# Optimization experiments

Hardware: AMD Instinct MI355X
Metric: run time of the kernel (lower is better)

Reference implementation:

```python
import jax, jax.numpy as jnp
import numpy as np

D_MODEL = 1024
NUM_HEADS = 16
D_K = D_MODEL // NUM_HEADS
THETA = 10000.0


def _rope(x, pos):
    # x: [H, B, S, D_K]; pos: [S] int. Interleaved-pair rotation (matrix-form RoPE).
    d2 = D_K // 2
    inv_freq = THETA ** (-(2.0 * jnp.arange(d2, dtype=jnp.float32)) / D_K)  # [d2]
    ang = pos.astype(jnp.float32)[:, None] * inv_freq[None, :]              # [S, d2]
    sin, cos = jnp.sin(ang), jnp.cos(ang)
    xr = x.reshape(*x.shape[:-1], d2, 2)
    x0, x1 = xr[..., 0], xr[..., 1]
    out0 = cos * x0 - sin * x1
    out1 = sin * x0 + cos * x1
    return jnp.stack([out0, out1], axis=-1).reshape(x.shape)


def setup_inputs() -> dict:
    key = jax.random.key(0)
    ks = jax.random.split(key, 5)
    scale = 1.0 / np.sqrt(D_MODEL)
    return {
        "x": jax.random.normal(ks[0], (4, 2048, D_MODEL), dtype=jnp.float32),
        "token_positions": jnp.arange(2048, dtype=jnp.int32),
        "Wq": jax.random.normal(ks[1], (D_MODEL, D_MODEL), dtype=jnp.float32) * scale,
        "Wk": jax.random.normal(ks[2], (D_MODEL, D_MODEL), dtype=jnp.float32) * scale,
        "Wv": jax.random.normal(ks[3], (D_MODEL, D_MODEL), dtype=jnp.float32) * scale,
        "Wo": jax.random.normal(ks[4], (D_MODEL, D_MODEL), dtype=jnp.float32) * scale,
    }


def reference(x, token_positions, Wq, Wk, Wv, Wo):
    B, S, D = x.shape
    H, dk = NUM_HEADS, D_K
    # Projections (Linear stores weight [out,in], applies x @ W.T)
    def proj(W):
        return (x @ W.T).reshape(B, S, H, dk).transpose(2, 0, 1, 3)  # [H,B,S,dk]
    q, k, v = proj(Wq), proj(Wk), proj(Wv)
    q = _rope(q, token_positions)
    k = _rope(k, token_positions)
    scores = jnp.einsum("hbsd,hbtd->hbst", q, k) / jnp.sqrt(jnp.float32(dk))
    causal = jnp.tril(jnp.ones((S, S), dtype=bool))
    scores = jnp.where(causal, scores, jnp.float32(-1e9))
    attn = jax.nn.softmax(scores, axis=-1)
    out = jnp.einsum("hbst,hbtd->hbsd", attn, v)       # [H,B,S,dk]
    out = out.transpose(1, 2, 0, 3).reshape(B, S, D)   # [B,S,D]
    return out @ Wo.T
```

## Files before the change

kernel.cpp:

```cpp
#include <hip/hip_runtime.h>

typedef __bf16 bf16;
typedef bf16 bf16x8 __attribute__((ext_vector_type(8)));
typedef bf16 bf16x4 __attribute__((ext_vector_type(4)));
typedef float floatx4 __attribute__((ext_vector_type(4)));

#define D_MODEL 1024
#define SEQ     2048
#define NB      4
#define NH      16
#define DKH     64
#define ROPE_L2 0.4152410118609203f

__device__ __forceinline__ floatx4 mfma16(bf16x8 a, bf16x8 b, floatx4 c) {
  return __builtin_amdgcn_mfma_f32_16x16x32_bf16(a, b, c, 0, 0, 0);
}

__device__ __forceinline__ void gload_lds16(void* lds_uniform, const void* gsrc) {
  __builtin_amdgcn_global_load_lds(
      (__attribute__((address_space(1))) unsigned int*)(void*)(gsrc),
      (__attribute__((address_space(3))) unsigned int*)lds_uniform,
      16, 0, 0);
}

__global__ __launch_bounds__(256) void cvt_all(
    const float4* __restrict__ x,
    const float4* __restrict__ wq, const float4* __restrict__ wk,
    const float4* __restrict__ wv, const float4* __restrict__ wo,
    bf16x4* __restrict__ xb,
    bf16x4* __restrict__ b0, bf16x4* __restrict__ b1,
    bf16x4* __restrict__ b2, bf16x4* __restrict__ b3,
    const int* __restrict__ tokpos, float2* __restrict__ ropetab) {
  const int i = blockIdx.x * 256 + threadIdx.x;
  if (i < (1 << 21) + (1 << 20)) {
    const float4* src;
    bf16x4* dst;
    int off;
    if (i < (1 << 21)) {
      src = x; dst = xb; off = i;
    } else {
      const int j = i - (1 << 21);
      const int widx = j >> 18;
      off = j & ((1 << 18) - 1);
      src = (widx == 0) ? wq : (widx == 1) ? wk : (widx == 2) ? wv : wo;
      dst = (widx == 0) ? b0 : (widx == 1) ? b1 : (widx == 2) ? b2 : b3;
    }
    const float4 v = src[off];
    bf16x4 o;
    o[0] = (bf16)v.x; o[1] = (bf16)v.y; o[2] = (bf16)v.z; o[3] = (bf16)v.w;
    dst[off] = o;
  } else {
    const int k = i - (1 << 21) - (1 << 20);
    const int s = k >> 5, i2 = k & 31;
    const float ang = (float)tokpos[s] * exp2f(-(float)i2 * ROPE_L2);
    float sn, cs;
    sincosf(ang, &sn, &cs);
    ropetab[k] = make_float2(sn, cs);
  }
}

#define QK_SRC_DECL(Aptr, Bq, Bk)                                              \
  const int c_0 = w * 64 + lane;                                               \
  const int row0_ = c_0 >> 2, seg0_ = (c_0 & 3) ^ ((row0_ >> 1) & 3);          \
  const int c_1 = c_0 + 256;                                                   \
  const int row1_ = c_1 >> 2, seg1_ = (c_1 & 3) ^ ((row1_ >> 1) & 3);          \
  const bf16* asrc0 = (Aptr) + (size_t)(bm + row0_) * D_MODEL + seg0_ * 8;     \
  const bf16* asrc1 = (Aptr) + (size_t)(bm + row1_) * D_MODEL + seg1_ * 8;     \
  const bf16* bqsrc0 = (Bq) + (size_t)(bn + row0_) * D_MODEL + seg0_ * 8;      \
  const bf16* bqsrc1 = (Bq) + (size_t)(bn + row1_) * D_MODEL + seg1_ * 8;      \
  const bf16* bksrc0 = (Bk) + (size_t)(bn + row0_) * D_MODEL + seg0_ * 8;      \
  const bf16* bksrc1 = (Bk) + (size_t)(bn + row1_) * D_MODEL + seg1_ * 8;     \
  const int gsw = (g ^ ((r >> 1) & 3)) * 8;

#define QKA(buf) ((char*)LDSBUF + (buf) * 8192)
#define QKQ(buf) ((char*)LDSBUF + 16384 + (buf) * 8192)
#define QKK(buf) ((char*)LDSBUF + 32768 + (buf) * 8192)

#define QK_STAGE(buf, kk)                                                      \
  gload_lds16(QKA(buf) + (w * 64) * 16, asrc0 + (kk));                         \
  gload_lds16(QKQ(buf) + (w * 64) * 16, bqsrc0 + (kk));                        \
  gload_lds16(QKK(buf) + (w * 64) * 16, bksrc0 + (kk));                        \
  gload_lds16(QKA(buf) + (w * 64 + 256) * 16, asrc1 + (kk));                   \
  gload_lds16(QKQ(buf) + (w * 64 + 256) * 16, bqsrc1 + (kk));                  \
  gload_lds16(QKK(buf) + (w * 64 + 256) * 16, bksrc1 + (kk));

#define ROPEW(mm, nn, CV, SC)                                                  \
  _Pragma("unroll")                                                            \
  for (int reg = 0; reg < 4; ++reg) {                                          \
    const int srow = mm * 16 + g * 4 + reg;                                    \
    const int c = wc * 64 + nn * 16 + r;                                       \
    const int s_ = (bm + wr * 64 + srow) & (SEQ - 1);                          \
    const int d_ = c & 63;                                                     \
    float v = CV[reg];                                                         \
    float pp = __shfl_xor(v, 1);                                               \
    const float2 sc2 = ropetab[s_ * 32 + (d_ >> 1)];                           \
    float res = ((d_ & 1) == 0) ? (sc2.y * v - sc2.x * pp)                     \
                                : (sc2.x * pp + sc2.y * v);                    \
    res *= SC;                                                                 \
    *(bf16*)((char*)LDSBUF + srow * 272 + c * 2) = (bf16)res;                  \
  }

#define QK_EPI(A00,A01,A02,A03,A10,A11,A12,A13,A20,A21,A22,A23,A30,A31,A32,A33,\
               dst0, SC)                                                       \
  _Pragma("unroll")                                                            \
  for (int p = 0; p < 2; ++p) {                                                \
    if (wr == p) {                                                             \
      ROPEW(0, 0, A00, SC) ROPEW(0, 1, A01, SC) ROPEW(0, 2, A02, SC)           \
      ROPEW(0, 3, A03, SC) ROPEW(1, 0, A10, SC) ROPEW(1, 1, A11, SC)           \
      ROPEW(1, 2, A12, SC) ROPEW(1, 3, A13, SC) ROPEW(2, 0, A20, SC)           \
      ROPEW(2, 1, A21, SC) ROPEW(2, 2, A22, SC) ROPEW(2, 3, A23, SC)           \
      ROPEW(3, 0, A30, SC) ROPEW(3, 1, A31, SC) ROPEW(3, 2, A32, SC)           \
      ROPEW(3, 3, A33, SC)                                                     \
    }                                                                          \
    __syncthreads();                                                           \
    const int s_r = tid >> 2, quad = tid & 3;                                  \
    const int grow = bm + p * 64 + s_r;                                        \
    const int b_ = grow >> 11, s_ = grow & (SEQ - 1);                          \
    const int h_ = hbase + (quad >> 1);                                        \
    bf16* dstp = (dst0) + ((size_t)(b_ * NH + h_) * SEQ + s_) * DKH +          \
                 (quad & 1) * 32;                                              \
    _Pragma("unroll")                                                          \
    for (int j = 0; j < 4; ++j)                                                \
      *(float4*)(dstp + j * 8) =                                               \
          *(const float4*)((char*)LDSBUF + s_r * 272 + quad * 64 + j * 16);    \
    __syncthreads();                                                           \
  }

__global__ __launch_bounds__(256, 2) void gemm_qk(
    const bf16* __restrict__ A,
    const bf16* __restrict__ Wq, const bf16* __restrict__ Wk,
    bf16* __restrict__ Qd, bf16* __restrict__ Kd,
    const float2* __restrict__ ropetab) {
  __shared__ __align__(16) char LDSBUF[49152];
  const int orig = (int)(blockIdx.x + (blockIdx.y << 3));
  const int l = (orig & 7) * 64 + (orig >> 3);
  const int bm = (l >> 3) * 128, bn = (l & 7) * 128;
  const int tid = threadIdx.x, lane = tid & 63, w = tid >> 6;
  const int wr = w >> 1, wc = w & 1;
  const int r = lane & 15, g = lane >> 4;

  floatx4 q00 = {}, q01 = {}, q02 = {}, q03 = {};
  floatx4 q10 = {}, q11 = {}, q12 = {}, q13 = {};
  floatx4 q20 = {}, q21 = {}, q22 = {}, q23 = {};
  floatx4 q30 = {}, q31 = {}, q32 = {}, q33 = {};
  floatx4 k00 = {}, k01 = {}, k02 = {}, k03 = {};
  floatx4 k10 = {}, k11 = {}, k12 = {}, k13 = {};
  floatx4 k20 = {}, k21 = {}, k22 = {}, k23 = {};
  floatx4 k30 = {}, k31 = {}, k32 = {}, k33 = {};

  QK_SRC_DECL(A, Wq, Wk)
  QK_STAGE(0, 0)
  __syncthreads();
  int cub = 0;
  for (int kt = 0; kt < 32; ++kt) {
    if (kt + 1 < 32) { QK_STAGE(cub ^ 1, (kt + 1) * 32) }
    const bf16* Abase = (const bf16*)QKA(cub) + (wr * 64 + r) * 32 + gsw;
    const bf16* Qbase = (const bf16*)QKQ(cub) + (wc * 64 + r) * 32 + gsw;
    const bf16* Kbase = (const bf16*)QKK(cub) + (wc * 64 + r) * 32 + gsw;
    bf16x8 a0 = *(const bf16x8*)(Abase + 0 * 512);
    bf16x8 a1 = *(const bf16x8*)(Abase + 1 * 512);
    bf16x8 a2 = *(const bf16x8*)(Abase + 2 * 512);
    bf16x8 a3 = *(const bf16x8*)(Abase + 3 * 512);
    bf16x8 bq0 = *(const bf16x8*)(Qbase + 0 * 512);
    bf16x8 bq1 = *(const bf16x8*)(Qbase + 1 * 512);
    bf16x8 bq2 = *(const bf16x8*)(Qbase + 2 * 512);
    bf16x8 bq3 = *(const bf16x8*)(Qbase + 3 * 512);
    bf16x8 bk0 = *(const bf16x8*)(Kbase + 0 * 512);
    bf16x8 bk1 = *(const bf16x8*)(Kbase + 1 * 512);
    bf16x8 bk2 = *(const bf16x8*)(Kbase + 2 * 512);
    bf16x8 bk3 = *(const bf16x8*)(Kbase + 3 * 512);
    __builtin_amdgcn_s_setprio(1);
    q00 = mfma16(a0, bq0, q00); q01 = mfma16(a0, bq1, q01);
    q02 = mfma16(a0, bq2, q02); q03 = mfma16(a0, bq3, q03);
    k00 = mfma16(a0, bk0, k00); k01 = mfma16(a0, bk1, k01);
    k02 = mfma16(a0, bk2, k02); k03 = mfma16(a0, bk3, k03);
    q10 = mfma16(a1, bq0, q10); q11 = mfma16(a1, bq1, q11);
    q12 = mfma16(a1, bq2, q12); q13 = mfma16(a1, bq3, q13);
    k10 = mfma16(a1, bk0, k10); k11 = mfma16(a1, bk1, k11);
    k12 = mfma16(a1, bk2, k12); k13 = mfma16(a1, bk3, k13);
    q20 = mfma16(a2, bq0, q20); q21 = mfma16(a2, bq1, q21);
    q22 = mfma16(a2, bq2, q22); q23 = mfma16(a2, bq3, q23);
    k20 = mfma16(a2, bk0, k20); k21 = mfma16(a2, bk1, k21);
    k22 = mfma16(a2, bk2, k22); k23 = mfma16(a2, bk3, k23);
    q30 = mfma16(a3, bq0, q30); q31 = mfma16(a3, bq1, q31);
    q32 = mfma16(a3, bq2, q32); q33 = mfma16(a3, bq3, q33);
    k30 = mfma16(a3, bk0, k30); k31 = mfma16(a3, bk1, k31);
    k32 = mfma16(a3, bk2, k32); k33 = mfma16(a3, bk3, k33);
    __builtin_amdgcn_s_setprio(0);
    __syncthreads();
    cub ^= 1;
  }

  const int hbase = bn >> 6;
  QK_EPI(q00,q01,q02,q03,q10,q11,q12,q13,q20,q21,q22,q23,q30,q31,q32,q33,
         Qd, 0.125f)
  QK_EPI(k00,k01,k02,k03,k10,k11,k12,k13,k20,k21,k22,k23,k30,k31,k32,k33,
         Kd, 1.0f)
}

#define GEMM_ACC_DECL                              \
  floatx4 c00 = {}, c01 = {}, c02 = {}, c03 = {};  \
  floatx4 c10 = {}, c11 = {}, c12 = {}, c13 = {};  \
  floatx4 c20 = {}, c21 = {}, c22 = {}, c23 = {};  \
  floatx4 c30 = {}, c31 = {}, c32 = {}, c33 = {};

#define AS_BASE(buf) ((char*)LDSBUF + (buf) * 8192)
#define BS_BASE(buf) ((char*)LDSBUF + 16384 + (buf) * 8192)

#define GEMM_STAGE(buf, kk)                                                    \
  gload_lds16(AS_BASE(buf) + (w * 64) * 16, asrc0 + (kk));                     \
  gload_lds16(BS_BASE(buf) + (w * 64) * 16, bsrc0 + (kk));                     \
  gload_lds16(AS_BASE(buf) + (w * 64 + 256) * 16, asrc1 + (kk));               \
  gload_lds16(BS_BASE(buf) + (w * 64 + 256) * 16, bsrc1 + (kk));

#define GEMM_MAINLOOP(Aptr, Bptr)                                              \
  const int c_0 = w * 64 + lane;                                               \
  const int row0_ = c_0 >> 2, seg0_ = (c_0 & 3) ^ ((row0_ >> 1) & 3);          \
  const int c_1 = c_0 + 256;                                                   \
  const int row1_ = c_1 >> 2, seg1_ = (c_1 & 3) ^ ((row1_ >> 1) & 3);          \
  const bf16* asrc0 = (Aptr) + (size_t)(bm + row0_) * D_MODEL + seg0_ * 8;     \
  const bf16* asrc1 = (Aptr) + (size_t)(bm + row1_) * D_MODEL + seg1_ * 8;     \
  const bf16* bsrc0 = (Bptr) + (size_t)(bn + row0_) * D_MODEL + seg0_ * 8;     \
  const bf16* bsrc1 = (Bptr) + (size_t)(bn + row1_) * D_MODEL + seg1_ * 8;     \
  const int gsw = (g ^ ((r >> 1) & 3)) * 8;                                    \
  GEMM_STAGE(0, 0)                                                             \
  __syncthreads();                                                             \
  int cub = 0;                                                                 \
  for (int kt = 0; kt < 32; ++kt) {                                            \
    if (kt + 1 < 32) { GEMM_STAGE(cub ^ 1, (kt + 1) * 32) }                    \
    const bf16* Abase = (const bf16*)AS_BASE(cub) + (wr * 64 + r) * 32 + gsw;  \
    const bf16* Bbase = (const bf16*)BS_BASE(cub) + (wc * 64 + r) * 32 + gsw;  \
    bf16x8 a0 = *(const bf16x8*)(Abase + 0 * 512);                             \
    bf16x8 a1 = *(const bf16x8*)(Abase + 1 * 512);                             \
    bf16x8 a2 = *(const bf16x8*)(Abase + 2 * 512);                             \
    bf16x8 a3 = *(const bf16x8*)(Abase + 3 * 512);                             \
    bf16x8 b0 = *(const bf16x8*)(Bbase + 0 * 512);                             \
    bf16x8 b1 = *(const bf16x8*)(Bbase + 1 * 512);                             \
    bf16x8 b2 = *(const bf16x8*)(Bbase + 2 * 512);                             \
    bf16x8 b3 = *(const bf16x8*)(Bbase + 3 * 512);                             \
    __builtin_amdgcn_s_setprio(1);                                             \
    c00 = mfma16(a0, b0, c00); c01 = mfma16(a0, b1, c01);                      \
    c02 = mfma16(a0, b2, c02); c03 = mfma16(a0, b3, c03);                      \
    c10 = mfma16(a1, b0, c10); c11 = mfma16(a1, b1, c11);                      \
    c12 = mfma16(a1, b2, c12); c13 = mfma16(a1, b3, c13);                      \
    c20 = mfma16(a2, b0, c20); c21 = mfma16(a2, b1, c21);                      \
    c22 = mfma16(a2, b2, c22); c23 = mfma16(a2, b3, c23);                      \
    c30 = mfma16(a3, b0, c30); c31 = mfma16(a3, b1, c31);                      \
    c32 = mfma16(a3, b2, c32); c33 = mfma16(a3, b3, c33);                      \
    __builtin_amdgcn_s_setprio(0);                                             \
    __syncthreads();                                                           \
    cub ^= 1;                                                                  \
  }

#define V_WRITE(mm, nn, CV)                                                    \
  _Pragma("unroll")                                                            \
  for (int reg = 0; reg < 4; ++reg) {                                          \
    const int crow = nn * 16 + r;                                              \
    const int s_l = wr * 64 + mm * 16 + g * 4 + reg;                           \
    *(bf16*)((char*)LDSBUF + crow * 272 + s_l * 2) = (bf16)CV[reg];            \
  }

__global__ __launch_bounds__(256, 3) void gemm_v(const bf16* __restrict__ A,
                                                 const bf16* __restrict__ Wv,
                                                 bf16* __restrict__ Vd) {
  __shared__ __align__(16) char LDSBUF[32768];
  const int orig = (int)(blockIdx.x + (blockIdx.y << 3));
  const int l = (orig & 7) * 64 + (orig >> 3);
  const int bm = (l >> 3) * 128, bn = (l & 7) * 128;
  const int tid = threadIdx.x, lane = tid & 63, w = tid >> 6;
  const int wr = w >> 1, wc = w & 1;
  const int r = lane & 15, g = lane >> 4;
  GEMM_ACC_DECL
  GEMM_MAINLOOP(A, Wv)

  const int hbase = bn >> 6;
  const int b_ = bm >> 11, sbase = bm & (SEQ - 1);
#pragma unroll
  for (int p = 0; p < 2; ++p) {
    if (wc == p) {
      V_WRITE(0, 0, c00) V_WRITE(0, 1, c01) V_WRITE(0, 2, c02) V_WRITE(0, 3, c03)
      V_WRITE(1, 0, c10) V_WRITE(1, 1, c11) V_WRITE(1, 2, c12) V_WRITE(1, 3, c13)
      V_WRITE(2, 0, c20) V_WRITE(2, 1, c21) V_WRITE(2, 2, c22) V_WRITE(2, 3, c23)
      V_WRITE(3, 0, c30) V_WRITE(3, 1, c31) V_WRITE(3, 2, c32) V_WRITE(3, 3, c33)
    }
    __syncthreads();
    const int c_r = tid >> 2, quad = tid & 3;
    const int c = p * 64 + c_r;
    const int h_ = hbase + (c >> 6), d_ = c & 63;
    bf16* dstp = Vd + ((size_t)(b_ * NH + h_) * DKH + d_) * SEQ + sbase + quad * 32;
#pragma unroll
    for (int j = 0; j < 4; ++j)
      *(float4*)(dstp + j * 8) =
          *(const float4*)((char*)LDSBUF + c_r * 272 + quad * 64 + j * 16);
    __syncthreads();
  }
}

#define OUT_EPI(mm, nn, CV)                                                    \
  _Pragma("unroll")                                                            \
  for (int reg = 0; reg < 4; ++reg) {                                          \
    const int grow = bm + wr * 64 + mm * 16 + g * 4 + reg;                     \
    const int gcol = bn + wc * 64 + nn * 16 + r;                               \
    C[(size_t)grow * D_MODEL + gcol] = CV[reg];                                \
  }

__global__ __launch_bounds__(256, 3) void gemm_out(const bf16* __restrict__ A,
                                                   const bf16* __restrict__ Bw,
                                                   float* __restrict__ C) {
  __shared__ __align__(16) char LDSBUF[32768];
  const int orig = (int)(blockIdx.x + (blockIdx.y << 3));
  const int l = (orig & 7) * 64 + (orig >> 3);
  const int bm = (l >> 3) * 128, bn = (l & 7) * 128;
  const int tid = threadIdx.x, lane = tid & 63, w = tid >> 6;
  const int wr = w >> 1, wc = w & 1;
  const int r = lane & 15, g = lane >> 4;
  GEMM_ACC_DECL
  GEMM_MAINLOOP(A, Bw)
  OUT_EPI(0, 0, c00) OUT_EPI(0, 1, c01) OUT_EPI(0, 2, c02) OUT_EPI(0, 3, c03)
  OUT_EPI(1, 0, c10) OUT_EPI(1, 1, c11) OUT_EPI(1, 2, c12) OUT_EPI(1, 3, c13)
  OUT_EPI(2, 0, c20) OUT_EPI(2, 1, c21) OUT_EPI(2, 2, c22) OUT_EPI(2, 3, c23)
  OUT_EPI(3, 0, c30) OUT_EPI(3, 1, c31) OUT_EPI(3, 2, c32) OUT_EPI(3, 3, c33)
}

__global__ __launch_bounds__(256, 3) void attn128(const bf16* __restrict__ Q,
                                                  const bf16* __restrict__ Kk,
                                                  const bf16* __restrict__ Vt,
                                                  bf16* __restrict__ AO) {
  const int orig = (int)(blockIdx.x + (blockIdx.y << 4));
  const int i_ = orig >> 3;
  const int qt = 15 - (i_ >> 3);
  const int bh = (orig & 7) * 8 + (i_ & 7);
  const int b = bh >> 4, h = bh & 15;
  const int tid = threadIdx.x, lane = tid & 63, w = tid >> 6;
  const int r = lane & 15, g = lane >> 4;
  const int q0 = qt * 128 + w * 32;

  const bf16* Qb = Q + (size_t)bh * SEQ * DKH;
  const bf16* Kb = Kk + (size_t)bh * SEQ * DKH;
  const bf16* Vb = Vt + (size_t)bh * DKH * SEQ;

  __shared__ bf16 Ks[2][64 * 64];
  __shared__ bf16 Vs[2][64 * 64];
  __shared__ bf16 Ps[4][32 * 64];

  int ldsoff[2];
  const char* ksrc[2];
  const char* vsrc[2];
#pragma unroll
  for (int j = 0; j < 2; ++j) {
    const int L = (w * 64 + lane + 256 * j) * 16;
    const int S = L ^ (((L >> 7) & 7) << 4);
    ldsoff[j] = (w * 64 + 256 * j) * 16;
    ksrc[j] = (const char*)Kb + S;
    vsrc[j] = (const char*)Vb + (size_t)(S >> 7) * (SEQ * 2) + (S & 127);
  }

#define ATTN_STAGE(buf, tt)                                                   \
  _Pragma("unroll")                                                           \
  for (int j = 0; j < 2; ++j) {                                               \
    gload_lds16((char*)Ks[buf] + ldsoff[j], ksrc[j] + (size_t)(tt) * 8192);   \
    gload_lds16((char*)Vs[buf] + ldsoff[j], vsrc[j] + (size_t)(tt) * 128);    \
  }

#define SM_TILE(MASKED)                                                        \
  _Pragma("unroll")                                                            \
  for (int m = 0; m < 2; ++m) {                                                \
    const int qq_ = q0 + m * 16 + r;                                           \
    const int wl_ = m * 16 + r;                                                \
    _Pragma("unroll")                                                          \
    for (int nf = 0; nf < 4; ++nf) {                                           \
      floatx4 p;                                                               \
      _Pragma("unroll")                                                        \
      for (int reg = 0; reg < 4; ++reg) {                                      \
        float pe = exp2f(fmaf(sc[m][nf][reg], 1.442695041f, -17.31234049f));   \
        if (MASKED && (t0 + nf * 16 + g * 4 + reg > qq_)) pe = 0.f;            \
        p[reg] = pe;                                                           \
      }                                                                        \
      l2[m] += p;                                                              \
      unsigned u0, u1;                                                         \
      asm("v_cvt_pk_bf16_f32 %0, %1, %2" : "=v"(u0) : "v"(p[0]), "v"(p[1]));   \
      asm("v_cvt_pk_bf16_f32 %0, %1, %2" : "=v"(u1) : "v"(p[2]), "v"(p[3]));   \
      const int pb = (wl_ * 128 + nf * 32 + g * 8) ^ ((wl_ & 7) << 4);         \
      *(uint2*)((char*)Ps[w] + pb) = make_uint2(u0, u1);                       \
    }                                                                          \
  }

  bf16x8 qf[2][2];
#pragma unroll
  for (int m = 0; m < 2; ++m)
#pragma unroll
    for (int ks = 0; ks < 2; ++ks)
      qf[m][ks] = *(const bf16x8*)(Qb + (size_t)(q0 + m * 16 + r) * DKH + ks * 32 + g * 8);

  floatx4 o[2][4] = {};
  floatx4 l2[2] = {};

  const int nt = 2 * qt + 2;
  ATTN_STAGE(0, 0)
  __syncthreads();
  int cu = 0;
  for (int t = 0; t < nt; ++t) {
    if (t + 1 < nt) ATTN_STAGE(cu ^ 1, t + 1)
    const int t0 = t * 64;

    floatx4 sc[2][4];
    __builtin_amdgcn_s_setprio(1);
#pragma unroll
    for (int nf = 0; nf < 4; ++nf) {
      const int row = nf * 16 + r;
      const int off0 = (row * 128 + g * 16) ^ ((row & 7) << 4);
      bf16x8 kf0 = *(const bf16x8*)((const char*)Ks[cu] + off0);
      bf16x8 kf1 = *(const bf16x8*)((const char*)Ks[cu] + (off0 ^ 64));
      sc[0][nf] = mfma16(kf1, qf[0][1], mfma16(kf0, qf[0][0], floatx4{0.f, 0.f, 0.f, 0.f}));
      sc[1][nf] = mfma16(kf1, qf[1][1], mfma16(kf0, qf[1][0], floatx4{0.f, 0.f, 0.f, 0.f}));
    }
    __builtin_amdgcn_s_setprio(0);

    const bool edge = (t0 + 63 > q0);
    if (edge) {
      SM_TILE(1)
    } else {
      SM_TILE(0)
    }
    asm volatile("s_waitcnt lgkmcnt(0)" ::: "memory");

    bf16x8 pf[2][2];
#pragma unroll
    for (int m = 0; m < 2; ++m)
#pragma unroll
      for (int ks = 0; ks < 2; ++ks) {
        const int prow = m * 16 + r;
        const int ab = (prow * 128 + ks * 64 + g * 16) ^ ((prow & 7) << 4);
        pf[m][ks] = *(const bf16x8*)((const char*)Ps[w] + ab);
      }
    __builtin_amdgcn_s_setprio(1);
#pragma unroll
    for (int nf = 0; nf < 4; ++nf) {
      const int vrow = nf * 16 + r;
      const int vb0 = (vrow * 128 + g * 16) ^ ((vrow & 7) << 4);
      bf16x8 vf0 = *(const bf16x8*)((const char*)Vs[cu] + vb0);
      bf16x8 vf1 = *(const bf16x8*)((const char*)Vs[cu] + (vb0 ^ 64));
#pragma unroll
      for (int m = 0; m < 2; ++m)
        o[m][nf] = mfma16(pf[m][1], vf1, mfma16(pf[m][0], vf0, o[m][nf]));
    }
    __builtin_amdgcn_s_setprio(0);
    __syncthreads();
    cu ^= 1;
  }

  float lsm[2];
#pragma unroll
  for (int m = 0; m < 2; ++m) {
    float ls = l2[m][0] + l2[m][1] + l2[m][2] + l2[m][3];
    ls += __shfl_xor(ls, 16);
    ls += __shfl_xor(ls, 32);
    lsm[m] = ls;
  }
  float linv[2][4];
#pragma unroll
  for (int m = 0; m < 2; ++m)
#pragma unroll
    for (int reg = 0; reg < 4; ++reg)
      linv[m][reg] = 1.f / __shfl(lsm[m], g * 4 + reg);

#pragma unroll
  for (int m = 0; m < 2; ++m)
#pragma unroll
    for (int nf = 0; nf < 4; ++nf)
#pragma unroll
      for (int reg = 0; reg < 4; ++reg) {
        const int s = q0 + m * 16 + g * 4 + reg;
        const int d = nf * 16 + r;
        const float val = o[m][nf][reg] * linv[m][reg];
        AO[((size_t)(b * SEQ + s)) * D_MODEL + h * DKH + d] = (bf16)val;
      }
}

extern "C" void kernel_launch(void* const* d_in, const int* in_sizes, int n_in,
                              void* d_out, int out_size, void* d_ws, size_t ws_size,
                              hipStream_t stream) {
  const float* x = (const float*)d_in[0];
  const int* tokpos = (const int*)d_in[1];
  const float* Wq = (const float*)d_in[2];
  const float* Wk = (const float*)d_in[3];
  const float* Wv = (const float*)d_in[4];
  const float* Wo = (const float*)d_in[5];
  float* out = (float*)d_out;

  char* ws = (char*)d_ws;
  if (ws_size < (72ull << 20)) return;

  bf16* xb  = (bf16*)(ws);
  bf16* wb0 = (bf16*)(ws + (16ull << 20));
  bf16* wb1 = (bf16*)(ws + (18ull << 20));
  bf16* wb2 = (bf16*)(ws + (20ull << 20));
  bf16* wb3 = (bf16*)(ws + (22ull << 20));
  bf16* Qb  = (bf16*)(ws + (24ull << 20));
  bf16* Kb  = (bf16*)(ws + (40ull << 20));
  bf16* Vt  = (bf16*)(ws + (56ull << 20));
  bf16* AO  = (bf16*)(ws);
  float2* ropetab = (float2*)d_out;

  cvt_all<<<12544, 256, 0, stream>>>((const float4*)x, (const float4*)Wq,
                                     (const float4*)Wk, (const float4*)Wv,
                                     (const float4*)Wo, (bf16x4*)xb,
                                     (bf16x4*)wb0, (bf16x4*)wb1,
                                     (bf16x4*)wb2, (bf16x4*)wb3,
                                     tokpos, ropetab);

  gemm_qk<<<dim3(8, 64), 256, 0, stream>>>(xb, wb0, wb1, Qb, Kb, ropetab);
  gemm_v<<<dim3(8, 64), 256, 0, stream>>>(xb, wb2, Vt);
  attn128<<<dim3(16, 64), 256, 0, stream>>>(Qb, Kb, Vt, AO);
  gemm_out<<<dim3(8, 64), 256, 0, stream>>>(AO, wb3, out);
}
```

Before: 174.9 us.

## Merge QK and V projection kernels; single-buffer V in attention for occupancy

The separate QK and V projection GEMMs become one launch that uses blockIdx.z to choose the branch. This removes a kernel launch and lets the V blocks run alongside the QK blocks. In attention, V is now held in a single LDS buffer and is loaded only after the PV matmul finishes, with an extra barrier before P·V. This cuts LDS so launch bounds can rise to 4 blocks, but V loads now overlap only the QK/softmax phase, and the extra syncs may stall. V blocks in the merged kernel also inherit the 49KB LDS and the launch bound of 2.

Result: slower. 205.1 us (+17.2%).

```diff
diff --git a/kernel.cpp b/kernel.cpp
--- a/kernel.cpp
+++ b/kernel.cpp
@@ -125,84 +125,6 @@
           *(const float4*)((char*)LDSBUF + s_r * 272 + quad * 64 + j * 16);    \
     __syncthreads();                                                           \
   }
-
-__global__ __launch_bounds__(256, 2) void gemm_qk(
-    const bf16* __restrict__ A,
-    const bf16* __restrict__ Wq, const bf16* __restrict__ Wk,
-    bf16* __restrict__ Qd, bf16* __restrict__ Kd,
-    const float2* __restrict__ ropetab) {
-  __shared__ __align__(16) char LDSBUF[49152];
-  const int orig = (int)(blockIdx.x + (blockIdx.y << 3));
-  const int l = (orig & 7) * 64 + (orig >> 3);
-  const int bm = (l >> 3) * 128, bn = (l & 7) * 128;
-  const int tid = threadIdx.x, lane = tid & 63, w = tid >> 6;
-  const int wr = w >> 1, wc = w & 1;
-  const int r = lane & 15, g = lane >> 4;
-
-  floatx4 q00 = {}, q01 = {}, q02 = {}, q03 = {};
-  floatx4 q10 = {}, q11 = {}, q12 = {}, q13 = {};
-  floatx4 q20 = {}, q21 = {}, q22 = {}, q23 = {};
-  floatx4 q30 = {}, q31 = {}, q32 = {}, q33 = {};
-  floatx4 k00 = {}, k01 = {}, k02 = {}, k03 = {};
-  floatx4 k10 = {}, k11 = {}, k12 = {}, k13 = {};
-  floatx4 k20 = {}, k21 = {}, k22 = {}, k23 = {};
-  floatx4 k30 = {}, k31 = {}, k32 = {}, k33 = {};
-
-  QK_SRC_DECL(A, Wq, Wk)
-  QK_STAGE(0, 0)
-  __syncthreads();
-  int cub = 0;
-  for (int kt = 0; kt < 32; ++kt) {
-    if (kt + 1 < 32) { QK_STAGE(cub ^ 1, (kt + 1) * 32) }
-    const bf16* Abase = (const bf16*)QKA(cub) + (wr * 64 + r) * 32 + gsw;
-    const bf16* Qbase = (const bf16*)QKQ(cub) + (wc * 64 + r) * 32 + gsw;
-    const bf16* Kbase = (const bf16*)QKK(cub) + (wc * 64 + r) * 32 + gsw;
-    bf16x8 a0 = *(const bf16x8*)(Abase + 0 * 512);
-    bf16x8 a1 = *(const bf16x8*)(Abase + 1 * 512);
-    bf16x8 a2 = *(const bf16x8*)(Abase + 2 * 512);
-    bf16x8 a3 = *(const bf16x8*)(Abase + 3 * 512);
-    bf16x8 bq0 = *(const bf16x8*)(Qbase + 0 * 512);
-    bf16x8 bq1 = *(const bf16x8*)(Qbase + 1 * 512);
-    bf16x8 bq2 = *(const bf16x8*)(Qbase + 2 * 512);
-    bf16x8 bq3 = *(const bf16x8*)(Qbase + 3 * 512);
-    bf16x8 bk0 = *(const bf16x8*)(Kbase + 0 * 512);
-    bf16x8 bk1 = *(const bf16x8*)(Kbase + 1 * 512);
-    bf16x8 bk2 = *(const bf16x8*)(Kbase + 2 * 512);
-    bf16x8 bk3 = *(const bf16x8*)(Kbase + 3 * 512);
-    __builtin_amdgcn_s_setprio(1);
-    q00 = mfma16(a0, bq0, q00); q01 = mfma16(a0, bq1, q01);
-    q02 = mfma16(a0, bq2, q02); q03 = mfma16(a0, bq3, q03);
-    k00 = mfma16(a0, bk0, k00); k01 = mfma16(a0, bk1, k01);
-    k02 = mfma16(a0, bk2, k02); k03 = mfma16(a0, bk3, k03);
-    q10 = mfma16(a1, bq0, q10); q11 = mfma16(a1, bq1, q11);
-    q12 = mfma16(a1, bq2, q12); q13 = mfma16(a1, bq3, q13);
-    k10 = mfma16(a1, bk0, k10); k11 = mfma16(a1, bk1, k11);
-    k12 = mfma16(a1, bk2, k12); k13 = mfma16(a1, bk3, k13);
-    q20 = mfma16(a2, bq0, q20); q21 = mfma16(a2, bq1, q21);
-    q22 = mfma16(a2, bq2, q22); q23 = mfma16(a2, bq3, q23);
-    k20 = mfma16(a2, bk0, k20); k21 = mfma16(a2, bk1, k21);
-    k22 = mfma16(a2, bk2, k22); k23 = mfma16(a2, bk3, k23);
-    q30 = mfma16(a3, bq0, q30); q31 = mfma16(a3, bq1, q31);
-    q32 = mfma16(a3, bq2, q32); q33 = mfma16(a3, bq3, q33);
-    k30 = mfma16(a3, bk0, k30); k31 = mfma16(a3, bk1, k31);
-    k32 = mfma16(a3, bk2, k32); k33 = mfma16(a3, bk3, k33);
-    __builtin_amdgcn_s_setprio(0);
-    __syncthreads();
-    cub ^= 1;
-  }
-
-  const int hbase = bn >> 6;
-  QK_EPI(q00,q01,q02,q03,q10,q11,q12,q13,q20,q21,q22,q23,q30,q31,q32,q33,
-         Qd, 0.125f)
-  QK_EPI(k00,k01,k02,k03,k10,k11,k12,k13,k20,k21,k22,k23,k30,k31,k32,k33,
-         Kd, 1.0f)
-}
-
-#define GEMM_ACC_DECL                              \
-  floatx4 c00 = {}, c01 = {}, c02 = {}, c03 = {};  \
-  floatx4 c10 = {}, c11 = {}, c12 = {}, c13 = {};  \
-  floatx4 c20 = {}, c21 = {}, c22 = {}, c23 = {};  \
-  floatx4 c30 = {}, c31 = {}, c32 = {}, c33 = {};
 
 #define AS_BASE(buf) ((char*)LDSBUF + (buf) * 8192)
 #define BS_BASE(buf) ((char*)LDSBUF + 16384 + (buf) * 8192)
@@ -260,39 +182,105 @@
     *(bf16*)((char*)LDSBUF + crow * 272 + s_l * 2) = (bf16)CV[reg];            \
   }
 
-__global__ __launch_bounds__(256, 3) void gemm_v(const bf16* __restrict__ A,
-                                                 const bf16* __restrict__ Wv,
-                                                 bf16* __restrict__ Vd) {
-  __shared__ __align__(16) char LDSBUF[32768];
+__global__ __launch_bounds__(256, 2) void gemm_proj(
+    const bf16* __restrict__ A,
+    const bf16* __restrict__ Wq, const bf16* __restrict__ Wk,
+    const bf16* __restrict__ Wv,
+    bf16* __restrict__ Qd, bf16* __restrict__ Kd, bf16* __restrict__ Vd,
+    const float2* __restrict__ ropetab) {
+  __shared__ __align__(16) char LDSBUF[49152];
   const int orig = (int)(blockIdx.x + (blockIdx.y << 3));
   const int l = (orig & 7) * 64 + (orig >> 3);
   const int bm = (l >> 3) * 128, bn = (l & 7) * 128;
   const int tid = threadIdx.x, lane = tid & 63, w = tid >> 6;
   const int wr = w >> 1, wc = w & 1;
   const int r = lane & 15, g = lane >> 4;
-  GEMM_ACC_DECL
-  GEMM_MAINLOOP(A, Wv)
-
   const int hbase = bn >> 6;
-  const int b_ = bm >> 11, sbase = bm & (SEQ - 1);
-#pragma unroll
-  for (int p = 0; p < 2; ++p) {
-    if (wc == p) {
-      V_WRITE(0, 0, c00) V_WRITE(0, 1, c01) V_WRITE(0, 2, c02) V_WRITE(0, 3, c03)
-      V_WRITE(1, 0, c10) V_WRITE(1, 1, c11) V_WRITE(1, 2, c12) V_WRITE(1, 3, c13)
-      V_WRITE(2, 0, c20) V_WRITE(2, 1, c21) V_WRITE(2, 2, c22) V_WRITE(2, 3, c23)
-      V_WRITE(3, 0, c30) V_WRITE(3, 1, c31) V_WRITE(3, 2, c32) V_WRITE(3, 3, c33)
+
+  if (blockIdx.z == 0) {
+    floatx4 q00 = {}, q01 = {}, q02 = {}, q03 = {};
+    floatx4 q10 = {}, q11 = {}, q12 = {}, q13 = {};
+    floatx4 q20 = {}, q21 = {}, q22 = {}, q23 = {};
+    floatx4 q30 = {}, q31 = {}, q32 = {}, q33 = {};
+    floatx4 k00 = {}, k01 = {}, k02 = {}, k03 = {};
+    floatx4 k10 = {}, k11 = {}, k12 = {}, k13 = {};
+    floatx4 k20 = {}, k21 = {}, k22 = {}, k23 = {};
+    floatx4 k30 = {}, k31 = {}, k32 = {}, k33 = {};
+
+    QK_SRC_DECL(A, Wq, Wk)
+    QK_STAGE(0, 0)
+    __syncthreads();
+    int cub = 0;
+    for (int kt = 0; kt < 32; ++kt) {
+      if (kt + 1 < 32) { QK_STAGE(cub ^ 1, (kt + 1) * 32) }
+      const bf16* Abase = (const bf16*)QKA(cub) + (wr * 64 + r) * 32 + gsw;
+      const bf16* Qbase = (const bf16*)QKQ(cub) + (wc * 64 + r) * 32 + gsw;
+      const bf16* Kbase = (const bf16*)QKK(cub) + (wc * 64 + r) * 32 + gsw;
+      bf16x8 a0 = *(const bf16x8*)(Abase + 0 * 512);
+      bf16x8 a1 = *(const bf16x8*)(Abase + 1 * 512);
+      bf16x8 a2 = *(const bf16x8*)(Abase + 2 * 512);
+      bf16x8 a3 = *(const bf16x8*)(Abase + 3 * 512);
+      bf16x8 bq0 = *(const bf16x8*)(Qbase + 0 * 512);
+      bf16x8 bq1 = *(const bf16x8*)(Qbase + 1 * 512);
+      bf16x8 bq2 = *(const bf16x8*)(Qbase + 2 * 512);
+      bf16x8 bq3 = *(const bf16x8*)(Qbase + 3 * 512);
+      bf16x8 bk0 = *(const bf16x8*)(Kbase + 0 * 512);
+      bf16x8 bk1 = *(const bf16x8*)(Kbase + 1 * 512);
+      bf16x8 bk2 = *(const bf16x8*)(Kbase + 2 * 512);
+      bf16x8 bk3 = *(const bf16x8*)(Kbase + 3 * 512);
+      __builtin_amdgcn_s_setprio(1);
+      q00 = mfma16(a0, bq0, q00); q01 = mfma16(a0, bq1, q01);
+      q02 = mfma16(a0, bq2, q02); q03 = mfma16(a0, bq3, q03);
+      k00 = mfma16(a0, bk0, k00); k01 = mfma16(a0, bk1, k01);
+      k02 = mfma16(a0, bk2, k02); k03 = mfma16(a0, bk3, k03);
+      q10 = mfma16(a1, bq0, q10); q11 = mfma16(a1, bq1, q11);
+      q12 = mfma16(a1, bq2, q12); q13 = mfma16(a1, bq3, q13);
+      k10 = mfma16(a1, bk0, k10); k11 = mfma16(a1, bk1, k11);
+      k12 = mfma16(a1, bk2, k12); k13 = mfma16(a1, bk3, k13);
+      q20 = mfma16(a2, bq0, q20); q21 = mfma16(a2, bq1, q21);
+      q22 = mfma16(a2, bq2, q22); q23 = mfma16(a2, bq3, q23);
+      k20 = mfma16(a2, bk0, k20); k21 = mfma16(a2, bk1, k21);
+      k22 = mfma16(a2, bk2, k22); k23 = mfma16(a2, bk3, k23);
+      q30 = mfma16(a3, bq0, q30); q31 = mfma16(a3, bq1, q31);
+      q32 = mfma16(a3, bq2, q32); q33 = mfma16(a3, bq3, q33);
+      k30 = mfma16(a3, bk0, k30); k31 = mfma16(a3, bk1, k31);
+      k32 = mfma16(a3, bk2, k32); k33 = mfma16(a3, bk3, k33);
+      __builtin_amdgcn_s_setprio(0);
+      __syncthreads();
+      cub ^= 1;
     }
-    __syncthreads();
-    const int c_r = tid >> 2, quad = tid & 3;
-    const int c = p * 64 + c_r;
-    const int h_ = hbase + (c >> 6), d_ = c & 63;
-    bf16* dstp = Vd + ((size_t)(b_ * NH + h_) * DKH + d_) * SEQ + sbase + quad * 32;
-#pragma unroll
-    for (int j = 0; j < 4; ++j)
-      *(float4*)(dstp + j * 8) =
-          *(const float4*)((char*)LDSBUF + c_r * 272 + quad * 64 + j * 16);
-    __syncthreads();
+
+    QK_EPI(q00,q01,q02,q03,q10,q11,q12,q13,q20,q21,q22,q23,q30,q31,q32,q33,
+           Qd, 0.125f)
+    QK_EPI(k00,k01,k02,k03,k10,k11,k12,k13,k20,k21,k22,k23,k30,k31,k32,k33,
+           Kd, 1.0f)
+  } else {
+    floatx4 c00 = {}, c01 = {}, c02 = {}, c03 = {};
+    floatx4 c10 = {}, c11 = {}, c12 = {}, c13 = {};
+    floatx4 c20 = {}, c21 = {}, c22 = {}, c23 = {};
+    floatx4 c30 = {}, c31 = {}, c32 = {}, c33 = {};
+    GEMM_MAINLOOP(A, Wv)
+
+    const int b_ = bm >> 11, sbase = bm & (SEQ - 1);
+#pragma unroll
+    for (int p = 0; p < 2; ++p) {
+      if (wc == p) {
+        V_WRITE(0, 0, c00) V_WRITE(0, 1, c01) V_WRITE(0, 2, c02) V_WRITE(0, 3, c03)
+        V_WRITE(1, 0, c10) V_WRITE(1, 1, c11) V_WRITE(1, 2, c12) V_WRITE(1, 3, c13)
+        V_WRITE(2, 0, c20) V_WRITE(2, 1, c21) V_WRITE(2, 2, c22) V_WRITE(2, 3, c23)
+        V_WRITE(3, 0, c30) V_WRITE(3, 1, c31) V_WRITE(3, 2, c32) V_WRITE(3, 3, c33)
+      }
+      __syncthreads();
+      const int c_r = tid >> 2, quad = tid & 3;
+      const int c = p * 64 + c_r;
+      const int h_ = hbase + (c >> 6), d_ = c & 63;
+      bf16* dstp = Vd + ((size_t)(b_ * NH + h_) * DKH + d_) * SEQ + sbase + quad * 32;
+#pragma unroll
+      for (int j = 0; j < 4; ++j)
+        *(float4*)(dstp + j * 8) =
+            *(const float4*)((char*)LDSBUF + c_r * 272 + quad * 64 + j * 16);
+      __syncthreads();
+    }
   }
 }
 
@@ -314,7 +302,10 @@
   const int tid = threadIdx.x, lane = tid & 63, w = tid >> 6;
   const int wr = w >> 1, wc = w & 1;
   const int r = lane & 15, g = lane >> 4;
-  GEMM_ACC_DECL
+  floatx4 c00 = {}, c01 = {}, c02 = {}, c03 = {};
+  floatx4 c10 = {}, c11 = {}, c12 = {}, c13 = {};
+  floatx4 c20 = {}, c21 = {}, c22 = {}, c23 = {};
+  floatx4 c30 = {}, c31 = {}, c32 = {}, c33 = {};
   GEMM_MAINLOOP(A, Bw)
   OUT_EPI(0, 0, c00) OUT_EPI(0, 1, c01) OUT_EPI(0, 2, c02) OUT_EPI(0, 3, c03)
   OUT_EPI(1, 0, c10) OUT_EPI(1, 1, c11) OUT_EPI(1, 2, c12) OUT_EPI(1, 3, c13)
@@ -322,7 +313,7 @@
   OUT_EPI(3, 0, c30) OUT_EPI(3, 1, c31) OUT_EPI(3, 2, c32) OUT_EPI(3, 3, c33)
 }
 
-__global__ __launch_bounds__(256, 3) void attn128(const bf16* __restrict__ Q,
+__global__ __launch_bounds__(256, 4) void attn128(const bf16* __restrict__ Q,
                                                   const bf16* __restrict__ Kk,
                                                   const bf16* __restrict__ Vt,
                                                   bf16* __restrict__ AO) {
@@ -340,7 +331,7 @@
   const bf16* Vb = Vt + (size_t)bh * DKH * SEQ;
 
   __shared__ bf16 Ks[2][64 * 64];
-  __shared__ bf16 Vs[2][64 * 64];
+  __shared__ bf16 Vs[64 * 64];
   __shared__ bf16 Ps[4][32 * 64];
 
   int ldsoff[2];
@@ -355,12 +346,15 @@
     vsrc[j] = (const char*)Vb + (size_t)(S >> 7) * (SEQ * 2) + (S & 127);
   }
 
-#define ATTN_STAGE(buf, tt)                                                   \
+#define STAGE_K(buf, tt)                                                      \
   _Pragma("unroll")                                                           \
-  for (int j = 0; j < 2; ++j) {                                               \
-    gload_lds16((char*)Ks[buf] + ldsoff[j], ksrc[j] + (size_t)(tt) * 8192);   \
-    gload_lds16((char*)Vs[buf] + ldsoff[j], vsrc[j] + (size_t)(tt) * 128);    \
-  }
+  for (int j = 0; j < 2; ++j)                                                 \
+    gload_lds16((char*)Ks[buf] + ldsoff[j], ksrc[j] + (size_t)(tt) * 8192);
+
+#define STAGE_V(tt)                                                           \
+  _Pragma("unroll")                                                           \
+  for (int j = 0; j < 2; ++j)                                                 \
+    gload_lds16((char*)Vs + ldsoff[j], vsrc[j] + (size_t)(tt) * 128);
 
 #define SM_TILE(MASKED)                                                        \
   _Pragma("unroll")                                                            \
@@ -396,11 +390,12 @@
   floatx4 l2[2] = {};
 
   const int nt = 2 * qt + 2;
-  ATTN_STAGE(0, 0)
+  STAGE_K(0, 0)
+  STAGE_V(0)
   __syncthreads();
   int cu = 0;
   for (int t = 0; t < nt; ++t) {
-    if (t + 1 < nt) ATTN_STAGE(cu ^ 1, t + 1)
+    if (t + 1 < nt) STAGE_K(cu ^ 1, t + 1)
     const int t0 = t * 64;
 
     floatx4 sc[2][4];
@@ -423,6 +418,7 @@
       SM_TILE(0)
     }
     asm volatile("s_waitcnt lgkmcnt(0)" ::: "memory");
+    __syncthreads();
 
     bf16x8 pf[2][2];
 #pragma unroll
@@ -438,14 +434,15 @@
     for (int nf = 0; nf < 4; ++nf) {
       const int vrow = nf * 16 + r;
       const int vb0 = (vrow * 128 + g * 16) ^ ((vrow & 7) << 4);
-      bf16x8 vf0 = *(const bf16x8*)((const char*)Vs[cu] + vb0);
-      bf16x8 vf1 = *(const bf16x8*)((const char*)Vs[cu] + (vb0 ^ 64));
+      bf16x8 vf0 = *(const bf16x8*)((const char*)Vs + vb0);
+      bf16x8 vf1 = *(const bf16x8*)((const char*)Vs + (vb0 ^ 64));
 #pragma unroll
       for (int m = 0; m < 2; ++m)
         o[m][nf] = mfma16(pf[m][1], vf1, mfma16(pf[m][0], vf0, o[m][nf]));
     }
     __builtin_amdgcn_s_setprio(0);
     __syncthreads();
+    if (t + 1 < nt) STAGE_V(t + 1)
     cu ^= 1;
   }
 
@@ -509,8 +506,8 @@
                                      (bf16x4*)wb2, (bf16x4*)wb3,
                                      tokpos, ropetab);
 
-  gemm_qk<<<dim3(8, 64), 256, 0, stream>>>(xb, wb0, wb1, Qb, Kb, ropetab);
-  gemm_v<<<dim3(8, 64), 256, 0, stream>>>(xb, wb2, Vt);
+  gemm_proj<<<dim3(8, 64, 2), 256, 0, stream>>>(xb, wb0, wb1, wb2,
+                                                Qb, Kb, Vt, ropetab);
   attn128<<<dim3(16, 64), 256, 0, stream>>>(Qb, Kb, Vt, AO);
   gemm_out<<<dim3(8, 64), 256, 0, stream>>>(AO, wb3, out);
 }
```
